# Performance work log

Hardware: AMD Instinct MI355X
Metric: run time of the kernel (lower is better)

Reference implementation:

```python
import jax, jax.numpy as jnp
import numpy as np

D_MODEL = 1024
N_HEADS = 16
MLP_DIM = 4096


def _layernorm(x, g, b, eps=1e-5):
    mu = jnp.mean(x, axis=-1, keepdims=True)
    var = jnp.var(x, axis=-1, keepdims=True)
    return (x - mu) * jax.lax.rsqrt(var + eps) * g + b


def setup_inputs() -> dict:
    key = jax.random.key(0)
    ks = jax.random.split(key, 12)
    B, S, D, F = 2, 2048, D_MODEL, MLP_DIM
    s = 1.0 / np.sqrt(D)
    sf = 1.0 / np.sqrt(F)
    return {
        "x": jax.random.normal(ks[0], (B, S, D), jnp.float32),
        "ln1_g": jnp.ones((D,), jnp.float32),
        "ln1_b": jnp.zeros((D,), jnp.float32),
        "w_q": jax.random.uniform(ks[1], (D, D), jnp.float32, -s, s),
        "w_k": jax.random.uniform(ks[2], (D, D), jnp.float32, -s, s),
        "w_v": jax.random.uniform(ks[3], (D, D), jnp.float32, -s, s),
        "w_o": jax.random.uniform(ks[4], (D, D), jnp.float32, -s, s),
        "b_o": jax.random.uniform(ks[5], (D,), jnp.float32, -s, s),
        "ln2_g": jnp.ones((D,), jnp.float32),
        "ln2_b": jnp.zeros((D,), jnp.float32),
        "w1": jax.random.uniform(ks[6], (D, F), jnp.float32, -s, s),
        "b1": jax.random.uniform(ks[7], (F,), jnp.float32, -s, s),
        "w2": jax.random.uniform(ks[8], (F, D), jnp.float32, -sf, sf),
        "b2": jax.random.uniform(ks[9], (D,), jnp.float32, -sf, sf),
    }


def reference(x, ln1_g, ln1_b, w_q, w_k, w_v, w_o, b_o, ln2_g, ln2_b, w1, b1, w2, b2):
    B, S, D = x.shape
    H = N_HEADS
    hd = D // H
    # --- attention sublayer (pre-LN, residual) ---
    h = _layernorm(x, ln1_g, ln1_b)
    q = (h @ w_q).reshape(B, S, H, hd).transpose(0, 2, 1, 3)  # [B,H,S,hd]
    k = (h @ w_k).reshape(B, S, H, hd).transpose(0, 2, 1, 3)
    v = (h @ w_v).reshape(B, S, H, hd).transpose(0, 2, 1, 3)
    scores = jnp.einsum('bhqd,bhkd->bhqk', q, k) / np.sqrt(hd)  # [B,H,S,S]
    attn = jax.nn.softmax(scores, axis=-1)
    out = jnp.einsum('bhqk,bhkd->bhqd', attn, v)
    out = out.transpose(0, 2, 1, 3).reshape(B, S, D)
    x = out @ w_o + b_o + x
    # --- MLP sublayer (pre-LN, residual) ---
    h = _layernorm(x, ln2_g, ln2_b)
    h = jax.nn.gelu(h @ w1 + b1, approximate=False)
    return h @ w2 + b2 + x
```

## Files before the change

kernel.cpp:

```cpp
#include <hip/hip_runtime.h>
#include <math.h>


typedef __attribute__((ext_vector_type(8))) short s8v;
typedef __attribute__((ext_vector_type(4))) short s4v;
typedef __attribute__((ext_vector_type(4))) float f4v;
typedef __attribute__((ext_vector_type(16))) float f16v;

#define M_ROWS 4096
#define DM 1024
#define FF 4096
#define QKV_LD 3072

__device__ inline short f2bf(float f) {
  unsigned u = __builtin_bit_cast(unsigned, f);
  u += 0x7fff + ((u >> 16) & 1);
  return (short)(u >> 16);
}
__device__ inline float bf2f(short s) {
  unsigned u = ((unsigned)(unsigned short)s) << 16;
  return __builtin_bit_cast(float, u);
}

__device__ inline void gload_lds16(const void* g, void* lds) {
  __builtin_amdgcn_global_load_lds(
      (const __attribute__((address_space(1))) unsigned*)(uintptr_t)g,
      (__attribute__((address_space(3))) unsigned*)(unsigned)(uintptr_t)lds,
      16, 0, 0);
}

__device__ inline s4v ds_tr16(unsigned off) {
  s4v r;
  asm volatile("ds_read_b64_tr_b16 %0, %1" : "=v"(r) : "v"(off));
  return r;
}

__device__ inline s8v cat8(s4v a, s4v b) {
  return __builtin_shufflevector(a, b, 0, 1, 2, 3, 4, 5, 6, 7);
}

__device__ inline unsigned pkbf(float a, float b) {
  unsigned r;
  asm("v_cvt_pk_bf16_f32 %0, %1, %2" : "=v"(r) : "v"(a), "v"(b));
  return r;
}

__device__ inline float gelu_t(float x) {
  float x3 = x * x * x;
  float z = fmaf(x3, 0.044715f, x) * 1.5957691216f;
  float e = __expf(z);
  float th = fmaf(-2.0f, __frcp_rn(e + 1.0f), 1.0f);
  return 0.5f * x * (1.0f + th);
}

__global__ void wt_kernel(const float* __restrict__ W, short* __restrict__ Wt,
                          int K, int N) {
  __shared__ float tile[32][33];
  int tx = threadIdx.x, ty = threadIdx.y;
  int n0 = blockIdx.x * 32, k0 = blockIdx.y * 32;
#pragma unroll
  for (int i = 0; i < 4; ++i)
    tile[ty + 8 * i][tx] = W[(size_t)(k0 + ty + 8 * i) * N + n0 + tx];
  __syncthreads();
#pragma unroll
  for (int i = 0; i < 4; ++i)
    Wt[(size_t)(n0 + ty + 8 * i) * K + k0 + tx] = f2bf(tile[tx][ty + 8 * i]);
}

__global__ __launch_bounds__(256) void ln_kernel(const float* __restrict__ x,
                                                 const float* __restrict__ g,
                                                 const float* __restrict__ b,
                                                 short* __restrict__ out) {
  int row = blockIdx.x, tid = threadIdx.x;
  const float4* xr = (const float4*)(x + (size_t)row * DM);
  float4 v = xr[tid];
  float s = v.x + v.y + v.z + v.w;
  float q = v.x * v.x + v.y * v.y + v.z * v.z + v.w * v.w;
#pragma unroll
  for (int off = 32; off; off >>= 1) {
    s += __shfl_down(s, off);
    q += __shfl_down(q, off);
  }
  __shared__ float red[8];
  if ((tid & 63) == 0) { red[tid >> 6] = s; red[4 + (tid >> 6)] = q; }
  __syncthreads();
  if (tid == 0) {
    float S = red[0] + red[1] + red[2] + red[3];
    float Q = red[4] + red[5] + red[6] + red[7];
    float mean = S * (1.0f / DM);
    float var = Q * (1.0f / DM) - mean * mean;
    red[0] = mean;
    red[1] = rsqrtf(var + 1e-5f);
  }
  __syncthreads();
  float mean = red[0], rstd = red[1];
  float4 gv = ((const float4*)g)[tid], bv = ((const float4*)b)[tid];
  s4v o;
  o[0] = f2bf((v.x - mean) * rstd * gv.x + bv.x);
  o[1] = f2bf((v.y - mean) * rstd * gv.y + bv.y);
  o[2] = f2bf((v.z - mean) * rstd * gv.z + bv.z);
  o[3] = f2bf((v.w - mean) * rstd * gv.w + bv.w);
  *(s4v*)&out[(size_t)row * DM + tid * 4] = o;
}

template <int EPI>
__global__ __launch_bounds__(256) void gemm_kernel(
    const short* __restrict__ A, const short* __restrict__ Bt,
    const float* __restrict__ bias, const float* __restrict__ res,
    void* __restrict__ Cout, int M, int N, int K) {
  __shared__ short As[2][128 * 64];
  __shared__ short Bs[2][128 * 64];
  int tid = threadIdx.x, lane = tid & 63, wave = tid >> 6;
  int wr = wave >> 1, wc = wave & 1;
  int l16 = lane & 15, lhi = lane >> 4;
  int row0 = blockIdx.y * 128, col0 = blockIdx.x * 128;
  int lrow = lane >> 3, lcol8 = (lane & 7) * 8;

  const f4v fzero = {0.f, 0.f, 0.f, 0.f};
  f4v acc[4][4];
#pragma unroll
  for (int m = 0; m < 4; ++m)
#pragma unroll
    for (int n = 0; n < 4; ++n) acc[m][n] = fzero;

  const int nt = K >> 6;

#pragma unroll
  for (int i = 0; i < 4; ++i) {
    int ch = wave * 4 + i;
    int row = ch * 8 + lrow;
    gload_lds16(&A[(size_t)(row0 + row) * K + lcol8], &As[0][ch * 512]);
    gload_lds16(&Bt[(size_t)(col0 + row) * K + lcol8], &Bs[0][ch * 512]);
  }
  __syncthreads();

  for (int t = 0; t < nt; ++t) {
    int cur = t & 1, nxt = cur ^ 1;
    if (t + 1 < nt) {
      int k1 = (t + 1) << 6;
#pragma unroll
      for (int i = 0; i < 4; ++i) {
        int ch = wave * 4 + i;
        int row = ch * 8 + lrow;
        gload_lds16(&A[(size_t)(row0 + row) * K + k1 + lcol8], &As[nxt][ch * 512]);
        gload_lds16(&Bt[(size_t)(col0 + row) * K + k1 + lcol8], &Bs[nxt][ch * 512]);
      }
    }
#pragma unroll
    for (int kk = 0; kk < 2; ++kk) {
      s8v af[4], bfr[4];
#pragma unroll
      for (int m = 0; m < 4; ++m)
        af[m] = *(const s8v*)&As[cur][(wr * 64 + m * 16 + l16) * 64 + kk * 32 + lhi * 8];
#pragma unroll
      for (int n = 0; n < 4; ++n)
        bfr[n] = *(const s8v*)&Bs[cur][(wc * 64 + n * 16 + l16) * 64 + kk * 32 + lhi * 8];
#pragma unroll
      for (int m = 0; m < 4; ++m)
#pragma unroll
        for (int n = 0; n < 4; ++n)
          acc[m][n] = __builtin_amdgcn_mfma_f32_16x16x32_bf16(af[m], bfr[n],
                                                              acc[m][n], 0, 0, 0);
    }
    __syncthreads();
  }

#pragma unroll
  for (int m = 0; m < 4; ++m)
#pragma unroll
    for (int n = 0; n < 4; ++n)
#pragma unroll
      for (int r = 0; r < 4; ++r) {
        int row = row0 + wr * 64 + m * 16 + lhi * 4 + r;
        int col = col0 + wc * 64 + n * 16 + l16;
        size_t idx = (size_t)row * N + col;
        float v = acc[m][n][r];
        if (EPI == 0) {
          ((short*)Cout)[idx] = f2bf(v);
        } else if (EPI == 1) {
          ((float*)Cout)[idx] = v + bias[col] + res[idx];
        } else {
          ((short*)Cout)[idx] = f2bf(gelu_t(v + bias[col]));
        }
      }
}

__global__ __launch_bounds__(512) void attn_kernel(const short* __restrict__ q,
                                                   const short* __restrict__ k,
                                                   const short* __restrict__ v,
                                                   short* __restrict__ opart,
                                                   float2* __restrict__ ml) {
  __shared__ short Ks[2][64 * 64];
  __shared__ short Vt[2][64 * 64];
  int tid = threadIdx.x, lane = tid & 63, w = tid >> 6;
  int l31 = lane & 31, l15 = lane & 15, h = lane >> 5;
  int qb = blockIdx.x * 256;
  int bh = blockIdx.y;
  int sp = blockIdx.z;
  int b = bh >> 4, hh = bh & 15;
  const size_t rbase = (size_t)b * 2048 * QKV_LD + (size_t)hh * 64;
  const float S2 = 0.18033688f;
  const int kbase = sp * 1024;

  int krow = w * 8 + (lane >> 3);
  int kcol = (((lane & 7) ^ (krow & 7)) * 8);
  int vnb = w >> 1, vrem = (w & 1) * 64 + lane;
  int vkey = vrem >> 1, vc8 = vrem & 1;

#define STAGE_KV(buf, kt)                                                      \
  {                                                                            \
    gload_lds16(&k[rbase + (size_t)((kt) + krow) * QKV_LD + kcol],             \
                &Ks[buf][w * 512]);                                            \
    gload_lds16(&v[rbase + (size_t)((kt) + vkey) * QKV_LD + vnb * 16 + vc8 * 8], \
                &Vt[buf][w * 512]);                                            \
  }

  int qrow = qb + w * 32 + l31;
  s8v qf[4];
#pragma unroll
  for (int c = 0; c < 4; ++c)
    qf[c] = *(const s8v*)&q[rbase + (size_t)qrow * QKV_LD + c * 16 + h * 8];

  f16v o0, o1;
#pragma unroll
  for (int i = 0; i < 16; ++i) { o0[i] = 0.f; o1[i] = 0.f; }
  float mreg = -3.0e38f, lsum = 0.f;

  STAGE_KV(0, kbase);
  __syncthreads();

  for (int t = 0; t < 16; ++t) {
    int cur = t & 1;
    if (t + 1 < 16) STAGE_KV(cur ^ 1, kbase + (t + 1) * 64);
    unsigned vtb = (unsigned)(uintptr_t)&Vt[cur][0];

    f16v t0, t1;
#pragma unroll
    for (int i = 0; i < 16; ++i) { t0[i] = 0.f; t1[i] = 0.f; }
    __builtin_amdgcn_s_setprio(1);
#pragma unroll
    for (int c = 0; c < 4; ++c) {
      int slot = ((2 * c + h) ^ (l31 & 7)) * 8;
      s8v k0f = *(const s8v*)&Ks[cur][l31 * 64 + slot];
      s8v k1f = *(const s8v*)&Ks[cur][(32 + l31) * 64 + slot];
      t0 = __builtin_amdgcn_mfma_f32_32x32x16_bf16(k0f, qf[c], t0, 0, 0, 0);
      t1 = __builtin_amdgcn_mfma_f32_32x32x16_bf16(k1f, qf[c], t1, 0, 0, 0);
    }
    __builtin_amdgcn_s_setprio(0);

    float mx[8];
#pragma unroll
    for (int i = 0; i < 8; ++i)
      mx[i] = fmaxf(fmaxf(t0[i], t0[i + 8]), fmaxf(t1[i], t1[i + 8]));
    float rm = fmaxf(fmaxf(fmaxf(mx[0], mx[1]), fmaxf(mx[2], mx[3])),
                     fmaxf(fmaxf(mx[4], mx[5]), fmaxf(mx[6], mx[7])));
    rm = fmaxf(rm, __shfl_xor(rm, 32));
    if (!__all(rm <= mreg + 64.0f)) {
      float newm = fmaxf(mreg, rm);
      float sc = exp2f((mreg - newm) * S2);
      mreg = newm;
#pragma unroll
      for (int i = 0; i < 16; ++i) { o0[i] *= sc; o1[i] *= sc; }
      lsum *= sc;
    }
    float ms2 = mreg * S2;
#pragma unroll
    for (int i = 0; i < 16; ++i) {
      t0[i] = exp2f(fmaf(t0[i], S2, -ms2));
      t1[i] = exp2f(fmaf(t1[i], S2, -ms2));
    }
    float sm[8];
#pragma unroll
    for (int i = 0; i < 8; ++i)
      sm[i] = (t0[i] + t0[i + 8]) + (t1[i] + t1[i + 8]);
    float rs = ((sm[0] + sm[1]) + (sm[2] + sm[3])) +
               ((sm[4] + sm[5]) + (sm[6] + sm[7]));
    rs += __shfl_xor(rs, 32);
    lsum += rs;

    s8v pB[4];
#pragma unroll
    for (int c = 0; c < 4; ++c) {
      int rb = (c & 1) * 8;
      float e0, e1, e2, e3, e4, e5, e6, e7;
      if (c < 2) {
        e0 = t0[rb]; e1 = t0[rb + 1]; e2 = t0[rb + 2]; e3 = t0[rb + 3];
        e4 = t0[rb + 4]; e5 = t0[rb + 5]; e6 = t0[rb + 6]; e7 = t0[rb + 7];
      } else {
        e0 = t1[rb]; e1 = t1[rb + 1]; e2 = t1[rb + 2]; e3 = t1[rb + 3];
        e4 = t1[rb + 4]; e5 = t1[rb + 5]; e6 = t1[rb + 6]; e7 = t1[rb + 7];
      }
      unsigned wA0 = pkbf(e0, e1), wA1 = pkbf(e2, e3);
      unsigned wB0 = pkbf(e4, e5), wB1 = pkbf(e6, e7);
      unsigned s0 = h ? wA0 : wB0, s1 = h ? wA1 : wB1;
      unsigned r0 = __shfl_xor(s0, 32), r1 = __shfl_xor(s1, 32);
      uint4 ww;
      ww.x = h ? r0 : wA0;
      ww.y = h ? r1 : wA1;
      ww.z = h ? wB0 : r0;
      ww.w = h ? wB1 : r1;
      pB[c] = __builtin_bit_cast(s8v, ww);
    }

    s4v va[2][4][2];
#pragma unroll
    for (int db = 0; db < 2; ++db) {
      unsigned base = vtb + (unsigned)(db * 2 + (l31 >> 4)) * 2048 + 2u * l15;
#pragma unroll
      for (int c = 0; c < 4; ++c) {
        unsigned a = base + (unsigned)(c * 512 + h * 256);
        va[db][c][0] = ds_tr16(a);
        va[db][c][1] = ds_tr16(a + 128);
      }
    }
    asm volatile("s_waitcnt lgkmcnt(0)");
    __builtin_amdgcn_sched_barrier(0);
    __builtin_amdgcn_s_setprio(1);
#pragma unroll
    for (int c = 0; c < 4; ++c) {
      o0 = __builtin_amdgcn_mfma_f32_32x32x16_bf16(cat8(va[0][c][0], va[0][c][1]),
                                                   pB[c], o0, 0, 0, 0);
      o1 = __builtin_amdgcn_mfma_f32_32x32x16_bf16(cat8(va[1][c][0], va[1][c][1]),
                                                   pB[c], o1, 0, 0, 0);
    }
    __builtin_amdgcn_s_setprio(0);
    __syncthreads();
  }

  size_t rowg = (size_t)b * 2048 + qrow;
  size_t obase = (size_t)sp * 4096 * 1024 + rowg * 1024 + hh * 64;
#pragma unroll
  for (int db = 0; db < 2; ++db)
#pragma unroll
    for (int qq = 0; qq < 4; ++qq) {
      s4v pv;
#pragma unroll
      for (int i = 0; i < 4; ++i)
        pv[i] = f2bf(db == 0 ? o0[qq * 4 + i] : o1[qq * 4 + i]);
      *(s4v*)&opart[obase + db * 32 + qq * 8 + h * 4] = pv;
    }
  if (h == 0) ml[(size_t)sp * 65536 + rowg * 16 + hh] = make_float2(mreg, lsum);
#undef STAGE_KV
}

__global__ __launch_bounds__(256) void attn_combine(const short* __restrict__ op,
                                                    const float2* __restrict__ ml,
                                                    short* __restrict__ o) {
  int row = blockIdx.x, t = threadIdx.x;
  int head = t >> 4;
  const float S2 = 0.18033688f;
  float2 ml0 = ml[(size_t)row * 16 + head];
  float2 ml1 = ml[65536 + (size_t)row * 16 + head];
  float M = fmaxf(ml0.x, ml1.x);
  float a0 = exp2f((ml0.x - M) * S2);
  float a1 = exp2f((ml1.x - M) * S2);
  float inv = 1.0f / fmaf(ml0.y, a0, ml1.y * a1);
  a0 *= inv; a1 *= inv;
  s4v v0 = *(const s4v*)&op[(size_t)row * 1024 + t * 4];
  s4v v1 = *(const s4v*)&op[(size_t)4096 * 1024 + row * 1024 + t * 4];
  s4v pv;
#pragma unroll
  for (int i = 0; i < 4; ++i)
    pv[i] = f2bf(bf2f(v0[i]) * a0 + bf2f(v1[i]) * a1);
  *(s4v*)&o[(size_t)row * 1024 + t * 4] = pv;
}

extern "C" void kernel_launch(void* const* d_in, const int* in_sizes, int n_in,
                              void* d_out, int out_size, void* d_ws, size_t ws_size,
                              hipStream_t stream) {
  (void)in_sizes; (void)n_in; (void)out_size; (void)ws_size;
  const float* x    = (const float*)d_in[0];
  const float* ln1g = (const float*)d_in[1];
  const float* ln1b = (const float*)d_in[2];
  const float* wq   = (const float*)d_in[3];
  const float* wk   = (const float*)d_in[4];
  const float* wv   = (const float*)d_in[5];
  const float* wo   = (const float*)d_in[6];
  const float* bo   = (const float*)d_in[7];
  const float* ln2g = (const float*)d_in[8];
  const float* ln2b = (const float*)d_in[9];
  const float* w1   = (const float*)d_in[10];
  const float* b1   = (const float*)d_in[11];
  const float* w2   = (const float*)d_in[12];
  const float* b2   = (const float*)d_in[13];
  float* out = (float*)d_out;

  char* ws = (char*)d_ws;
  const size_t MB = 1024 * 1024;
  short* h1   = (short*)(ws);
  short* qkv  = (short*)(ws + 8 * MB);
  short* mid  = (short*)(ws);
  short* at   = (short*)(ws + 32 * MB);
  short* h2   = (short*)(ws + 32 * MB);
  float* x2   = (float*)(ws + 40 * MB);
  short* opart = (short*)(ws + 40 * MB);
  float2* mlb  = (float2*)(ws);
  short* wqkvT = (short*)(ws + 56 * MB);
  short* wqT  = wqkvT;
  short* wkT  = wqkvT + 1024 * 1024;
  short* wvT  = wqkvT + 2 * 1024 * 1024;
  short* woT  = (short*)(ws + 62 * MB);
  short* w1T  = (short*)(ws + 64 * MB);
  short* w2T  = (short*)(ws + 72 * MB);

  dim3 tb(32, 8);
  wt_kernel<<<dim3(32, 32), tb, 0, stream>>>(wq, wqT, 1024, 1024);
  wt_kernel<<<dim3(32, 32), tb, 0, stream>>>(wk, wkT, 1024, 1024);
  wt_kernel<<<dim3(32, 32), tb, 0, stream>>>(wv, wvT, 1024, 1024);
  wt_kernel<<<dim3(32, 32), tb, 0, stream>>>(wo, woT, 1024, 1024);
  wt_kernel<<<dim3(128, 32), tb, 0, stream>>>(w1, w1T, 1024, 4096);
  wt_kernel<<<dim3(32, 128), tb, 0, stream>>>(w2, w2T, 4096, 1024);

  ln_kernel<<<M_ROWS, 256, 0, stream>>>(x, ln1g, ln1b, h1);

  gemm_kernel<0><<<dim3(24, 32), 256, 0, stream>>>(h1, wqkvT, nullptr, nullptr,
                                                   qkv, M_ROWS, QKV_LD, DM);

  attn_kernel<<<dim3(8, 32, 2), 512, 0, stream>>>(qkv, qkv + 1024, qkv + 2048,
                                                  opart, mlb);
  attn_combine<<<4096, 256, 0, stream>>>(opart, mlb, at);

  gemm_kernel<1><<<dim3(8, 32), 256, 0, stream>>>(at, woT, bo, x, x2, M_ROWS, DM, DM);

  ln_kernel<<<M_ROWS, 256, 0, stream>>>(x2, ln2g, ln2b, h2);

  gemm_kernel<2><<<dim3(32, 32), 256, 0, stream>>>(h2, w1T, b1, nullptr, mid,
                                                   M_ROWS, FF, DM);

  gemm_kernel<1><<<dim3(8, 32), 256, 0, stream>>>(mid, w2T, b2, x2, out,
                                                  M_ROWS, DM, FF);
}
```

Before: 276.9 us.

## Swizzle GEMM workgroup order and use partial vmcnt waits for prefetch overlap

Remaps the linear workgroup id across 8 groups so that consecutively dispatched blocks land on different XCDs with neighbouring tiles. It also replaces the full __syncthreads with explicit s_waitcnt vmcnt(8) plus s_barrier, so the current tile is consumed while the next tile's async global-to-LDS loads stay in flight. The aim is better cache locality and more overlap of loads with MFMA compute. The manual waitcnt counting depends on the number of outstanding loads per stage, and the swizzle assumes the grid size is divisible by 8.

```diff
diff --git a/kernel.cpp b/kernel.cpp
--- a/kernel.cpp
+++ b/kernel.cpp
@@ -113,7 +113,13 @@
   int tid = threadIdx.x, lane = tid & 63, wave = tid >> 6;
   int wr = wave >> 1, wc = wave & 1;
   int l16 = lane & 15, lhi = lane >> 4;
-  int row0 = blockIdx.y * 128, col0 = blockIdx.x * 128;
+
+  int nbx = gridDim.x;
+  int nwg = nbx * gridDim.y;
+  int orig = blockIdx.y * nbx + blockIdx.x;
+  int wgid = (orig & 7) * (nwg >> 3) + (orig >> 3);
+  int row0 = (wgid / nbx) * 128, col0 = (wgid % nbx) * 128;
+
   int lrow = lane >> 3, lcol8 = (lane & 7) * 8;
 
   const f4v fzero = {0.f, 0.f, 0.f, 0.f};
@@ -125,27 +131,31 @@
 
   const int nt = K >> 6;
 
-#pragma unroll
-  for (int i = 0; i < 4; ++i) {
-    int ch = wave * 4 + i;
-    int row = ch * 8 + lrow;
-    gload_lds16(&A[(size_t)(row0 + row) * K + lcol8], &As[0][ch * 512]);
-    gload_lds16(&Bt[(size_t)(col0 + row) * K + lcol8], &Bs[0][ch * 512]);
-  }
-  __syncthreads();
+#define G_STAGE(buf, kt)                                                       \
+  {                                                                            \
+    _Pragma("unroll")                                                          \
+    for (int i = 0; i < 4; ++i) {                                              \
+      int ch = wave * 4 + i;                                                   \
+      int row = ch * 8 + lrow;                                                 \
+      gload_lds16(&A[(size_t)(row0 + row) * K + (kt) + lcol8],                 \
+                  &As[buf][ch * 512]);                                         \
+      gload_lds16(&Bt[(size_t)(col0 + row) * K + (kt) + lcol8],                \
+                  &Bs[buf][ch * 512]);                                         \
+    }                                                                          \
+  }
+
+  G_STAGE(0, 0);
 
   for (int t = 0; t < nt; ++t) {
     int cur = t & 1, nxt = cur ^ 1;
     if (t + 1 < nt) {
-      int k1 = (t + 1) << 6;
-#pragma unroll
-      for (int i = 0; i < 4; ++i) {
-        int ch = wave * 4 + i;
-        int row = ch * 8 + lrow;
-        gload_lds16(&A[(size_t)(row0 + row) * K + k1 + lcol8], &As[nxt][ch * 512]);
-        gload_lds16(&Bt[(size_t)(col0 + row) * K + k1 + lcol8], &Bs[nxt][ch * 512]);
-      }
-    }
+      G_STAGE(nxt, (t + 1) << 6);
+      asm volatile("s_waitcnt vmcnt(8)");
+    } else {
+      asm volatile("s_waitcnt vmcnt(0)");
+    }
+    __builtin_amdgcn_sched_barrier(0);
+    __builtin_amdgcn_s_barrier();
 #pragma unroll
     for (int kk = 0; kk < 2; ++kk) {
       s8v af[4], bfr[4];
@@ -162,8 +172,11 @@
           acc[m][n] = __builtin_amdgcn_mfma_f32_16x16x32_bf16(af[m], bfr[n],
                                                               acc[m][n], 0, 0, 0);
     }
-    __syncthreads();
-  }
+    asm volatile("s_waitcnt lgkmcnt(0)");
+    __builtin_amdgcn_sched_barrier(0);
+    __builtin_amdgcn_s_barrier();
+  }
+#undef G_STAGE
 
 #pragma unroll
   for (int m = 0; m < 4; ++m)
```

New measurement: 280.0 us. About the same (+1.1%).

## Add 256x256-tile 512-thread GEMM kernel with swizzled LDS for MLP up-projection

Applied to the files above, without the earlier changes.

Introduces a new GEMM kernel using 256x256 output tiles, 8 waves per block, double-buffered async global-to-LDS loads with an XOR-swizzled LDS layout, and raised wave priority around the MFMA block. The FFN up-projection with GELU epilogue switches to it, launching 256 blocks instead of 1024. Larger tiles raise arithmetic intensity and cut redundant global loads. The cost is 128KB of LDS per block and high register pressure, so occupancy drops to one block per CU, and 256 blocks give under one wave of work on a 256-CU device.

```diff
diff --git a/kernel.cpp b/kernel.cpp
--- a/kernel.cpp
+++ b/kernel.cpp
@@ -172,6 +172,100 @@
 #pragma unroll
       for (int r = 0; r < 4; ++r) {
         int row = row0 + wr * 64 + m * 16 + lhi * 4 + r;
+        int col = col0 + wc * 64 + n * 16 + l16;
+        size_t idx = (size_t)row * N + col;
+        float v = acc[m][n][r];
+        if (EPI == 0) {
+          ((short*)Cout)[idx] = f2bf(v);
+        } else if (EPI == 1) {
+          ((float*)Cout)[idx] = v + bias[col] + res[idx];
+        } else {
+          ((short*)Cout)[idx] = f2bf(gelu_t(v + bias[col]));
+        }
+      }
+}
+
+template <int EPI>
+__global__ __launch_bounds__(512) void gemm256_kernel(
+    const short* __restrict__ A, const short* __restrict__ Bt,
+    const float* __restrict__ bias, const float* __restrict__ res,
+    void* __restrict__ Cout, int M, int N, int K) {
+  __shared__ short As[2][256 * 64];
+  __shared__ short Bs[2][256 * 64];
+  int tid = threadIdx.x, lane = tid & 63, w = tid >> 6;
+  int wr = w >> 2, wc = w & 3;
+  int l16 = lane & 15, lhi = lane >> 4;
+  int row0 = blockIdx.y * 256, col0 = blockIdx.x * 256;
+  int srow = lane >> 3, sg = lane & 7;
+  int scol = (sg ^ srow) * 8;
+
+  const f4v fzero = {0.f, 0.f, 0.f, 0.f};
+  f4v acc[8][4];
+#pragma unroll
+  for (int m = 0; m < 8; ++m)
+#pragma unroll
+    for (int n = 0; n < 4; ++n) acc[m][n] = fzero;
+
+  const int nt = K >> 6;
+
+#define G_STAGE256(buf, kt)                                                    \
+  {                                                                            \
+    _Pragma("unroll")                                                          \
+    for (int i = 0; i < 4; ++i) {                                              \
+      int rA = w * 32 + i * 8 + srow;                                          \
+      int dst = (w * 32 + i * 8) * 64;                                         \
+      gload_lds16(&A[(size_t)(row0 + rA) * K + (kt) + scol], &As[buf][dst]);   \
+      gload_lds16(&Bt[(size_t)(col0 + rA) * K + (kt) + scol], &Bs[buf][dst]);  \
+    }                                                                          \
+  }
+
+  G_STAGE256(0, 0);
+
+  for (int t = 0; t < nt; ++t) {
+    int cur = t & 1, nxt = cur ^ 1;
+    if (t + 1 < nt) {
+      G_STAGE256(nxt, (t + 1) << 6);
+      asm volatile("s_waitcnt vmcnt(8)" ::: "memory");
+    } else {
+      asm volatile("s_waitcnt vmcnt(0)" ::: "memory");
+    }
+    __builtin_amdgcn_sched_barrier(0);
+    __builtin_amdgcn_s_barrier();
+#pragma unroll
+    for (int kk = 0; kk < 2; ++kk) {
+      s8v af[8], bfr[4];
+#pragma unroll
+      for (int m = 0; m < 8; ++m) {
+        int r = wr * 128 + m * 16 + l16;
+        af[m] = *(const s8v*)&As[cur][r * 64 + ((kk * 4 + lhi) ^ (l16 & 7)) * 8];
+      }
+#pragma unroll
+      for (int n = 0; n < 4; ++n) {
+        int r = wc * 64 + n * 16 + l16;
+        bfr[n] = *(const s8v*)&Bs[cur][r * 64 + ((kk * 4 + lhi) ^ (l16 & 7)) * 8];
+      }
+      __builtin_amdgcn_s_setprio(1);
+#pragma unroll
+      for (int m = 0; m < 8; ++m)
+#pragma unroll
+        for (int n = 0; n < 4; ++n)
+          acc[m][n] = __builtin_amdgcn_mfma_f32_16x16x32_bf16(af[m], bfr[n],
+                                                              acc[m][n], 0, 0, 0);
+      __builtin_amdgcn_s_setprio(0);
+    }
+    asm volatile("s_waitcnt lgkmcnt(0)" ::: "memory");
+    __builtin_amdgcn_sched_barrier(0);
+    __builtin_amdgcn_s_barrier();
+  }
+#undef G_STAGE256
+
+#pragma unroll
+  for (int m = 0; m < 8; ++m)
+#pragma unroll
+    for (int n = 0; n < 4; ++n)
+#pragma unroll
+      for (int r = 0; r < 4; ++r) {
+        int row = row0 + wr * 128 + m * 16 + lhi * 4 + r;
         int col = col0 + wc * 64 + n * 16 + l16;
         size_t idx = (size_t)row * N + col;
         float v = acc[m][n][r];
@@ -424,8 +518,8 @@
 
   ln_kernel<<<M_ROWS, 256, 0, stream>>>(x2, ln2g, ln2b, h2);
 
-  gemm_kernel<2><<<dim3(32, 32), 256, 0, stream>>>(h2, w1T, b1, nullptr, mid,
-                                                   M_ROWS, FF, DM);
+  gemm256_kernel<2><<<dim3(16, 16), 512, 0, stream>>>(h2, w1T, b1, nullptr, mid,
+                                                      M_ROWS, FF, DM);
 
   gemm_kernel<1><<<dim3(8, 32), 256, 0, stream>>>(mid, w2T, b2, x2, out,
                                                   M_ROWS, DM, FF);
```

Measured after the change: 268.5 us. 1.03x faster.

## Add 256x256-tile 8-wave phased GEMM kernel for the MLP up-projection

Applied to the files above, without the earlier changes.

Adds a new GEMM kernel with 256x256 output tiles, 512 threads (8 waves), and four compute phases per K-step. Each phase issues the global-to-LDS loads for the next tile, then runs its MFMAs at raised priority between barriers. It replaces the 128x128 GEMM for the w1 up-projection with the GELU epilogue. The aim is more data reuse per tile and better overlap of memory traffic with MFMA work. In exchange the grid shrinks to 256 blocks on a chip with many CUs, and the kernel uses much more LDS and registers per block.

```diff
diff --git a/kernel.cpp b/kernel.cpp
--- a/kernel.cpp
+++ b/kernel.cpp
@@ -173,6 +173,113 @@
       for (int r = 0; r < 4; ++r) {
         int row = row0 + wr * 64 + m * 16 + lhi * 4 + r;
         int col = col0 + wc * 64 + n * 16 + l16;
+        size_t idx = (size_t)row * N + col;
+        float v = acc[m][n][r];
+        if (EPI == 0) {
+          ((short*)Cout)[idx] = f2bf(v);
+        } else if (EPI == 1) {
+          ((float*)Cout)[idx] = v + bias[col] + res[idx];
+        } else {
+          ((short*)Cout)[idx] = f2bf(gelu_t(v + bias[col]));
+        }
+      }
+}
+
+template <int EPI>
+__global__ __launch_bounds__(512, 2) void gemm8p_kernel(
+    const short* __restrict__ A, const short* __restrict__ Bt,
+    const float* __restrict__ bias, const float* __restrict__ res,
+    void* __restrict__ Cout, int M, int N, int K) {
+  __shared__ short As[2][2][128 * 64];
+  __shared__ short Bs[2][2][128 * 64];
+  int tid = threadIdx.x, lane = tid & 63, w = tid >> 6;
+  int wr = w >> 2, wc = w & 3;
+  int l16 = lane & 15, lhi = lane >> 4;
+  int row0 = blockIdx.y * 256, col0 = blockIdx.x * 256;
+  int srow = lane >> 3;
+  int scol = ((lane & 7) ^ srow) * 8;
+
+  const f4v fzero = {0.f, 0.f, 0.f, 0.f};
+  f4v acc[8][4];
+#pragma unroll
+  for (int m = 0; m < 8; ++m)
+#pragma unroll
+    for (int n = 0; n < 4; ++n) acc[m][n] = fzero;
+
+  const int nt = K >> 6;
+
+#define STG_A(dbuf, half, kt)                                                 \
+  { _Pragma("unroll") for (int j = 0; j < 2; ++j)                             \
+      gload_lds16(&A[(size_t)(row0 + (half) * 128 + (j * 8 + w) * 8 + srow) * K \
+                     + (kt) + scol],                                          \
+                  &As[dbuf][half][(j * 8 + w) * 512]); }
+#define STG_B(dbuf, half, kt)                                                 \
+  { _Pragma("unroll") for (int j = 0; j < 2; ++j)                             \
+      gload_lds16(&Bt[(size_t)(col0 + (half) * 128 + (j * 8 + w) * 8 + srow) * K \
+                      + (kt) + scol],                                         \
+                  &Bs[dbuf][half][(j * 8 + w) * 512]); }
+
+  STG_A(0, 0, 0); STG_B(0, 0, 0); STG_B(0, 1, 0); STG_A(0, 1, 0);
+  asm volatile("s_waitcnt vmcnt(0)" ::: "memory");
+  __builtin_amdgcn_sched_barrier(0);
+  __builtin_amdgcn_s_barrier();
+
+  for (int T = 0; T < nt; ++T) {
+    int d = T & 1, d1 = d ^ 1;
+    int ktn = (T + 1 < nt) ? ((T + 1) << 6) : 0;
+
+#define PHASE(p)                                                              \
+    {                                                                         \
+      const int mh = (p) >> 1, nh = (p) & 1;                                  \
+      s8v af[4][2], bf[2][2];                                                 \
+      _Pragma("unroll") for (int m2 = 0; m2 < 4; ++m2) {                      \
+        int rr = wr * 64 + m2 * 16 + l16;                                     \
+        _Pragma("unroll") for (int kk = 0; kk < 2; ++kk)                      \
+          af[m2][kk] = *(const s8v*)&As[d][mh]                                \
+              [rr * 64 + (((kk * 4 + lhi) ^ (rr & 7)) * 8)];                  \
+      }                                                                       \
+      _Pragma("unroll") for (int n2 = 0; n2 < 2; ++n2) {                      \
+        int rr = wc * 32 + n2 * 16 + l16;                                     \
+        _Pragma("unroll") for (int kk = 0; kk < 2; ++kk)                      \
+          bf[n2][kk] = *(const s8v*)&Bs[d][nh]                                \
+              [rr * 64 + (((kk * 4 + lhi) ^ (rr & 7)) * 8)];                  \
+      }                                                                       \
+      if ((p) == 0) STG_A(d1, 0, ktn);                                        \
+      if ((p) == 1) STG_B(d1, 0, ktn);                                        \
+      if ((p) == 2) STG_B(d1, 1, ktn);                                        \
+      if ((p) == 3) STG_A(d1, 1, ktn);                                        \
+      if ((p) != 2) asm volatile("s_waitcnt vmcnt(4)" ::: "memory");          \
+      __builtin_amdgcn_sched_barrier(0);                                      \
+      __builtin_amdgcn_s_barrier();                                           \
+      asm volatile("s_waitcnt lgkmcnt(0)" ::: "memory");                      \
+      __builtin_amdgcn_sched_barrier(0);                                      \
+      __builtin_amdgcn_s_setprio(1);                                          \
+      _Pragma("unroll") for (int kk = 0; kk < 2; ++kk)                        \
+        _Pragma("unroll") for (int m2 = 0; m2 < 4; ++m2)                      \
+          _Pragma("unroll") for (int n2 = 0; n2 < 2; ++n2)                    \
+            acc[mh * 4 + m2][nh * 2 + n2] =                                   \
+                __builtin_amdgcn_mfma_f32_16x16x32_bf16(                      \
+                    af[m2][kk], bf[n2][kk], acc[mh * 4 + m2][nh * 2 + n2],    \
+                    0, 0, 0);                                                 \
+      __builtin_amdgcn_s_setprio(0);                                          \
+      __builtin_amdgcn_sched_barrier(0);                                      \
+      __builtin_amdgcn_s_barrier();                                           \
+    }
+    PHASE(0) PHASE(1) PHASE(2) PHASE(3)
+#undef PHASE
+  }
+  asm volatile("s_waitcnt vmcnt(0)" ::: "memory");
+#undef STG_A
+#undef STG_B
+
+#pragma unroll
+  for (int m = 0; m < 8; ++m)
+#pragma unroll
+    for (int n = 0; n < 4; ++n)
+#pragma unroll
+      for (int r = 0; r < 4; ++r) {
+        int row = row0 + (m >> 2) * 128 + wr * 64 + (m & 3) * 16 + lhi * 4 + r;
+        int col = col0 + (n >> 1) * 128 + wc * 32 + (n & 1) * 16 + l16;
         size_t idx = (size_t)row * N + col;
         float v = acc[m][n][r];
         if (EPI == 0) {
@@ -424,8 +531,8 @@
 
   ln_kernel<<<M_ROWS, 256, 0, stream>>>(x2, ln2g, ln2b, h2);
 
-  gemm_kernel<2><<<dim3(32, 32), 256, 0, stream>>>(h2, w1T, b1, nullptr, mid,
-                                                   M_ROWS, FF, DM);
+  gemm8p_kernel<2><<<dim3(16, 16), 512, 0, stream>>>(h2, w1T, b1, nullptr, mid,
+                                                     M_ROWS, FF, DM);
 
   gemm_kernel<1><<<dim3(8, 32), 256, 0, stream>>>(mid, w2T, b2, x2, out,
                                                   M_ROWS, DM, FF);
```

New measurement: 271.1 us. -2.1%, faster.
